# Optimization experiments

Hardware: AMD Instinct MI355X
Metric: run time of the kernel (lower is better)

The kernel has to match this reference:

```python
import jax, jax.numpy as jnp
import numpy as np

B, H, N, D, M = 1, 4, 2048, 64, 256  # batch, heads, seq, dim_heads, nb_features
EPS = 1e-4


def _gaussian_orthogonal_random_matrix(nb_rows, nb_cols, seed=0):
    # scaling=1 path of the torch code: stacked transposed-Q orthogonal blocks,
    # scaled by sqrt(nb_cols).
    rng = np.random.default_rng(seed)
    blocks = []
    for _ in range(nb_rows // nb_cols):
        q, _ = np.linalg.qr(rng.standard_normal((nb_cols, nb_cols)))
        blocks.append(q.T)
    final = np.concatenate(blocks, axis=0)  # [nb_rows, nb_cols]
    return jnp.asarray(np.sqrt(float(nb_cols)) * final, dtype=jnp.float32)


def setup_inputs() -> dict:
    key = jax.random.key(0)
    kq, kk, kv = jax.random.split(key, 3)
    return {
        "q": jax.random.normal(kq, (B, H, N, D), dtype=jnp.float32),
        "k": jax.random.normal(kk, (B, H, N, D), dtype=jnp.float32),
        "v": jax.random.normal(kv, (B, H, N, D), dtype=jnp.float32),
        "projection_matrix": _gaussian_orthogonal_random_matrix(M, D),
    }


def _softmax_kernel(data, projection_matrix, is_query):
    # data: [B,H,N,D], projection_matrix: [M,D] -> features [B,H,N,M]
    data_normalizer = 1.0 / data.shape[-1] ** 0.25
    ratio = 1.0 / projection_matrix.shape[0] ** 0.5
    data_dash = jnp.einsum("bhnd,md->bhnm", data_normalizer * data, projection_matrix)
    diag_data = jnp.sum(data * data, axis=-1) * 0.5 * data_normalizer ** 2  # [B,H,N]
    diag_data = diag_data[..., None]  # [B,H,N,1]
    if is_query:
        stab = jnp.max(data_dash, axis=-1, keepdims=True)
    else:
        stab = jnp.max(data_dash)
    return ratio * (jnp.exp(data_dash - diag_data - stab) + EPS)


def _causal_linear_attention(q, k, v):
    # q,k: [B,H,N,M] features; v: [B,H,N,E]
    k_cumsum = jnp.cumsum(k, axis=-2)                       # [B,H,N,M]
    context = jnp.einsum("bhnm,bhne->bhnme", k, v)          # outer products
    context = jnp.cumsum(context, axis=-3)                  # cumulative over n
    context = context / k_cumsum[..., None]                 # [B,H,N,M,E]
    return jnp.einsum("bhnme,bhnm->bhne", context, q)


def reference(q, k, v, projection_matrix):
    q_feat = _softmax_kernel(q, projection_matrix, is_query=True)
    k_feat = _softmax_kernel(k, projection_matrix, is_query=False)
    return _causal_linear_attention(q_feat, k_feat, v)
```

## Files before the change

kernel.cpp:

```cpp
#include <hip/hip_runtime.h>
#include <math.h>

#define NH   4
#define SEQ  2048
#define DH   64
#define NF   256
#define ROWS (NH*SEQ)
#define DN    0.35355339059327373f
#define DIAGC 0.0625f
#define RATIO 0.0625f
#define EPSF  1e-4f

typedef __attribute__((ext_vector_type(8))) short bf8;
typedef __attribute__((ext_vector_type(4))) short bf4;
typedef __attribute__((ext_vector_type(4))) float f4;

static __device__ __forceinline__ unsigned short f2bf(float x) {
  union { float f; unsigned u; } v; v.f = x;
  unsigned r = v.u + 0x7FFF + ((v.u >> 16) & 1);
  return (unsigned short)(r >> 16);
}
static __device__ __forceinline__ float bf2f(unsigned short b) {
  union { unsigned u; float f; } v; v.u = ((unsigned)b) << 16;
  return v.f;
}

__global__ __launch_bounds__(256) void k_proj(const float* __restrict__ q,
    const float* __restrict__ k, const float* __restrict__ v,
    const float* __restrict__ P,
    unsigned short* __restrict__ qfb, float* __restrict__ dshd,
    float* __restrict__ bmax, unsigned short* __restrict__ vtb) {
  __shared__ float lds[64*65];
  const int b = blockIdx.x;
  if (b >= 1024) {
    const int cb = b - 1024;
    const int h = cb >> 5, n0 = (cb & 31) * 64;
    const int tid = threadIdx.x;
    for (int i = tid; i < 4096; i += 256) {
      int n = i >> 6, e = i & 63;
      lds[n*65 + e] = v[((size_t)h*SEQ + n0 + n)*DH + e];
    }
    __syncthreads();
    for (int i = tid; i < 4096; i += 256) {
      int e = i >> 6, n = i & 63;
      vtb[((size_t)h*DH + e)*SEQ + n0 + n] = f2bf(lds[n*65 + e]);
    }
    return;
  }
  const bool isq = b < 512;
  const int tile = isq ? b : b - 512;
  const int w = threadIdx.x >> 6, lane = threadIdx.x & 63;
  const int lr = lane & 15, g = lane >> 4;
  const float* x = (isq ? q : k) + (size_t)tile*16*DH;

  f4 a  = *(const f4*)(x + lr*DH + g*8);
  f4 bb = *(const f4*)(x + lr*DH + g*8 + 4);
  f4 c  = *(const f4*)(x + lr*DH + 32 + g*8);
  f4 d  = *(const f4*)(x + lr*DH + 32 + g*8 + 4);
  float ss = 0.f;
#pragma unroll
  for (int i = 0; i < 4; ++i) ss += a[i]*a[i] + bb[i]*bb[i] + c[i]*c[i] + d[i]*d[i];
  ss += __shfl_xor(ss, 16);
  ss += __shfl_xor(ss, 32);

  bf8 xh0, xh1, xl0, xl1;
#pragma unroll
  for (int i = 0; i < 4; ++i) {
    float v0 = DN*a[i], v1 = DN*bb[i], v2 = DN*c[i], v3 = DN*d[i];
    unsigned short h0 = f2bf(v0), h1 = f2bf(v1), h2 = f2bf(v2), h3 = f2bf(v3);
    xh0[i] = (short)h0; xh0[i+4] = (short)h1;
    xh1[i] = (short)h2; xh1[i+4] = (short)h3;
    xl0[i]   = (short)f2bf(v0 - bf2f(h0)); xl0[i+4] = (short)f2bf(v1 - bf2f(h1));
    xl1[i]   = (short)f2bf(v2 - bf2f(h2)); xl1[i+4] = (short)f2bf(v3 - bf2f(h3));
  }

  const int ct0 = w*4;
  f4 dsh[4];
#pragma unroll
  for (int cc = 0; cc < 4; ++cc) {
    const int ct = ct0 + cc;
    const float* prow = P + (ct*16 + lr)*DH + g*8;
    f4 p0 = *(const f4*)(prow);
    f4 p1 = *(const f4*)(prow + 4);
    f4 p2 = *(const f4*)(prow + 32);
    f4 p3 = *(const f4*)(prow + 36);
    bf8 bh0, bl0, bh1, bl1;
#pragma unroll
    for (int i = 0; i < 4; ++i) {
      unsigned short h0 = f2bf(p0[i]), h1 = f2bf(p1[i]);
      unsigned short h2 = f2bf(p2[i]), h3 = f2bf(p3[i]);
      bh0[i] = (short)h0; bh0[i+4] = (short)h1;
      bh1[i] = (short)h2; bh1[i+4] = (short)h3;
      bl0[i]   = (short)f2bf(p0[i] - bf2f(h0)); bl0[i+4] = (short)f2bf(p1[i] - bf2f(h1));
      bl1[i]   = (short)f2bf(p2[i] - bf2f(h2)); bl1[i+4] = (short)f2bf(p3[i] - bf2f(h3));
    }
    f4 acc = {0.f, 0.f, 0.f, 0.f};
    acc = __builtin_amdgcn_mfma_f32_16x16x32_bf16(xh0, bh0, acc, 0, 0, 0);
    acc = __builtin_amdgcn_mfma_f32_16x16x32_bf16(xh1, bh1, acc, 0, 0, 0);
    acc = __builtin_amdgcn_mfma_f32_16x16x32_bf16(xh0, bl0, acc, 0, 0, 0);
    acc = __builtin_amdgcn_mfma_f32_16x16x32_bf16(xh1, bl1, acc, 0, 0, 0);
    acc = __builtin_amdgcn_mfma_f32_16x16x32_bf16(xl0, bh0, acc, 0, 0, 0);
    acc = __builtin_amdgcn_mfma_f32_16x16x32_bf16(xl1, bh1, acc, 0, 0, 0);
    dsh[cc] = acc;
  }

  f4 mr;
#pragma unroll
  for (int r = 0; r < 4; ++r)
    mr[r] = fmaxf(fmaxf(dsh[0][r], dsh[1][r]), fmaxf(dsh[2][r], dsh[3][r]));
#pragma unroll
  for (int mk = 1; mk <= 8; mk <<= 1) {
#pragma unroll
    for (int r = 0; r < 4; ++r) mr[r] = fmaxf(mr[r], __shfl_xor(mr[r], mk));
  }
  if (lr == 0) {
#pragma unroll
    for (int r = 0; r < 4; ++r) lds[w*16 + 4*g + r] = mr[r];
  }
  __syncthreads();
  float rm[4], sr[4];
#pragma unroll
  for (int r = 0; r < 4; ++r) {
    rm[r] = fmaxf(fmaxf(lds[0*16 + 4*g + r], lds[1*16 + 4*g + r]),
                  fmaxf(lds[2*16 + 4*g + r], lds[3*16 + 4*g + r]));
    sr[r] = __shfl(ss, 4*g + r);
  }

  if (isq) {
    unsigned short* ob = qfb + (size_t)tile*16*NF;
#pragma unroll
    for (int cc = 0; cc < 4; ++cc) {
#pragma unroll
      for (int r = 0; r < 4; ++r)
        ob[(4*g + r)*NF + (ct0 + cc)*16 + lr] =
            f2bf(RATIO*(expf(dsh[cc][r] - (sr[r]*DIAGC + rm[r])) + EPSF));
    }
  } else {
    float* db = dshd + (size_t)tile*16*NF;
#pragma unroll
    for (int cc = 0; cc < 4; ++cc) {
#pragma unroll
      for (int r = 0; r < 4; ++r)
        db[(4*g + r)*NF + (ct0 + cc)*16 + lr] = dsh[cc][r] - sr[r]*DIAGC;
    }
    if (w == 0 && lr == 0) {
#pragma unroll
      for (int r = 0; r < 4; ++r) bmax[tile*16 + 4*g + r] = mr[r];
    }
  }
}

__global__ __launch_bounds__(256) void k_feat2(const float* __restrict__ dshd,
    const float* __restrict__ bmax, unsigned short* __restrict__ kfb,
    unsigned short* __restrict__ kft, float* __restrict__ csum) {
  const int u = blockIdx.x, m = threadIdx.x;
  const int h = u >> 7, t = u & 127;
  __shared__ float red[256];
  float mx = -3.4e38f;
  for (int i = m; i < ROWS; i += 256) mx = fmaxf(mx, bmax[i]);
  red[m] = mx;
  __syncthreads();
  for (int s = 128; s > 0; s >>= 1) {
    if (m < s) red[m] = fmaxf(red[m], red[m+s]);
    __syncthreads();
  }
  const float gg = red[0];
  const float* db = dshd + (size_t)u*16*NF + m;
  unsigned short* ob = kfb + (size_t)u*16*NF + m;
  float run = 0.f;
  bf8 k0, k1;
#pragma unroll
  for (int r = 0; r < 16; ++r) {
    unsigned short bv = f2bf(RATIO*(expf(db[r*NF] - gg) + EPSF));
    ob[r*NF] = bv;
    if (r < 8) k0[r] = (short)bv; else k1[r-8] = (short)bv;
    run += bf2f(bv);
  }
  csum[(size_t)u*NF + m] = run;
  unsigned short* kt = kft + ((size_t)(h*NF + m))*SEQ + t*16;
  *(bf8*)kt = k0;
  *(bf8*)(kt + 8) = k1;
}

__global__ __launch_bounds__(64) void k_state_build(
    const unsigned short* __restrict__ vtb, const unsigned short* __restrict__ kft,
    float* __restrict__ stateP) {
  const int lane = threadIdx.x;
  const int lr = lane & 15, g = lane >> 4;
  const int c = blockIdx.x >> 2, mtg = blockIdx.x & 3;
  const int h = blockIdx.y;
  f4 acc[4][4];
#pragma unroll
  for (int et = 0; et < 4; ++et)
#pragma unroll
    for (int mt = 0; mt < 4; ++mt) acc[et][mt] = (f4){0.f,0.f,0.f,0.f};

#pragma unroll
  for (int ks = 0; ks < 4; ++ks) {
    const int j0 = c*128 + ks*32 + g*8;
    bf8 xv[4], ym[4];
#pragma unroll
    for (int et = 0; et < 4; ++et)
      xv[et] = *(const bf8*)(vtb + ((size_t)(h*DH + et*16 + lr))*SEQ + j0);
#pragma unroll
    for (int mt = 0; mt < 4; ++mt)
      ym[mt] = *(const bf8*)(kft + ((size_t)(h*NF + (4*mtg + mt)*16 + lr))*SEQ + j0);
#pragma unroll
    for (int et = 0; et < 4; ++et)
#pragma unroll
      for (int mt = 0; mt < 4; ++mt)
        acc[et][mt] = __builtin_amdgcn_mfma_f32_16x16x32_bf16(xv[et], ym[mt], acc[et][mt], 0, 0, 0);
  }
  float* sp = stateP + (size_t)(h*16 + c)*64*NF;
#pragma unroll
  for (int et = 0; et < 4; ++et)
#pragma unroll
    for (int mt = 0; mt < 4; ++mt)
#pragma unroll
      for (int r = 0; r < 4; ++r)
        sp[(size_t)(et*16 + 4*g + r)*NF + (4*mtg + mt)*16 + lr] = acc[et][mt][r];
}

__global__ __launch_bounds__(64) void k_state_scan(const float* __restrict__ stateP,
    unsigned short* __restrict__ sthi, unsigned short* __restrict__ stlo,
    float* __restrict__ csum) {
  const int h = blockIdx.y;
  if (blockIdx.x == 64) {
    const int m0 = threadIdx.x * 4;
    f4 run = {0.f, 0.f, 0.f, 0.f};
#pragma unroll 4
    for (int c = 0; c < 128; ++c) {
      float* p = csum + ((size_t)(h*128 + c))*NF + m0;
      f4 x = *(const f4*)p;
      *(f4*)p = run;
      run += x;
    }
    return;
  }
  const int e = blockIdx.x;
  const int m0 = threadIdx.x * 4;
  f4 run = {0.f, 0.f, 0.f, 0.f};
  for (int c = 0; c < 16; ++c) {
    const size_t idx = (size_t)((h*16 + c)*64 + e)*NF + m0;
    unsigned short hi[4], lo[4];
#pragma unroll
    for (int i = 0; i < 4; ++i) {
      hi[i] = f2bf(run[i]);
      lo[i] = f2bf(run[i] - bf2f(hi[i]));
    }
    *(bf4*)(sthi + idx) = *(bf4*)hi;
    *(bf4*)(stlo + idx) = *(bf4*)lo;
    run += *(const f4*)(stateP + idx);
  }
}

__global__ __launch_bounds__(128) void k_attn3(const unsigned short* __restrict__ qpb,
                                               const unsigned short* __restrict__ kfb,
                                               const unsigned short* __restrict__ vtb,
                                               const unsigned short* __restrict__ sthi,
                                               const unsigned short* __restrict__ stlo,
                                               const float* __restrict__ csum,
                                               float* __restrict__ out) {
  const int h = blockIdx.y;
  const int b = blockIdx.x;
  const int c = b >> 2, qt = b & 3;
  const int tid = threadIdx.x;
  const int wid = tid >> 6, lane = tid & 63;
  const int t = c*8 + qt*2 + wid;
  const int lr = lane & 15, g = lane >> 4;
  const int jc0 = c*8;
  const int nstage = qt*2 + 2;

  __shared__ __align__(16) char smem[26624];
  char* Ks = smem + 16384;
  char* Vs = smem + 24576;

  {
    const int u = h*128 + t;
    f4 run = *(const f4*)(csum + (size_t)u*NF + lane*4);
    const unsigned short* kfp = kfb + ((size_t)(h*SEQ + t*16))*NF + lane*4;
    const unsigned short* qfp = qpb + ((size_t)(h*SEQ + t*16))*NF + lane*4;
#pragma unroll
    for (int r = 0; r < 16; ++r) {
      bf4 kv = *(const bf4*)(kfp + (size_t)r*NF);
      bf4 qv = *(const bf4*)(qfp + (size_t)r*NF);
      unsigned short qp[4];
#pragma unroll
      for (int i = 0; i < 4; ++i) {
        run[i] += bf2f((unsigned short)kv[i]);
        qp[i] = f2bf(bf2f((unsigned short)qv[i]) / run[i]);
      }
      const int rloc = wid*16 + r;
      const int byte = (rloc*512 + lane*8) ^ ((rloc & 7) << 4);
      *(bf4*)(smem + byte) = *(bf4*)qp;
    }
  }
  __syncthreads();

  bf8 qf[8];
  {
    const int rloc = wid*16 + lr;
#pragma unroll
    for (int kb = 0; kb < 8; ++kb) {
      const int byte = (rloc*512 + g*16 + kb*64) ^ ((rloc & 7) << 4);
      qf[kb] = *(const bf8*)(smem + byte);
    }
  }

  const char* kTile = (const char*)(kfb + (size_t)h*SEQ*NF);
  const char* vTile = (const char*)(vtb + (size_t)h*DH*SEQ);

  const int ko0 = wid*4096 +    0 + lane*16;
  const int ko1 = wid*4096 + 1024 + lane*16;
  const int ko2 = wid*4096 + 2048 + lane*16;
  const int ko3 = wid*4096 + 3072 + lane*16;
  const int kw0 = ko0 ^ (((ko0 >> 9) & 7) << 4);
  const int kw1 = ko1 ^ (((ko1 >> 9) & 7) << 4);
  const int kw2 = ko2 ^ (((ko2 >> 9) & 7) << 4);
  const int kw3 = ko3 ^ (((ko3 >> 9) & 7) << 4);
  const int vo = tid*16;
  const int ve = vo >> 5;
  const int vn = vo & 31;

  f4 sk0, sk1, sk2, sk3, sv;
  {
    const char* kt = kTile + (size_t)jc0*8192;
    sk0 = *(const f4*)(kt + ko0);
    sk1 = *(const f4*)(kt + ko1);
    sk2 = *(const f4*)(kt + ko2);
    sk3 = *(const f4*)(kt + ko3);
    sv  = *(const f4*)(vTile + (size_t)ve*4096 + (size_t)jc0*32 + vn);
  }

  f4 o0 = {0,0,0,0}, o1 = {0,0,0,0}, o2 = {0,0,0,0}, o3 = {0,0,0,0};
  {
    const unsigned short* SH = sthi + ((size_t)((h*16 + c)*64 + lr))*NF + g*8;
    const unsigned short* SL = stlo + ((size_t)((h*16 + c)*64 + lr))*NF + g*8;
#pragma unroll
    for (int ks = 0; ks < 8; ++ks) {
#pragma unroll
      for (int et = 0; et < 4; ++et) {
        bf8 bh = *(const bf8*)(SH + et*16*NF + ks*32);
        bf8 bl = *(const bf8*)(SL + et*16*NF + ks*32);
        f4 acc = (et == 0) ? o0 : (et == 1) ? o1 : (et == 2) ? o2 : o3;
        acc = __builtin_amdgcn_mfma_f32_16x16x32_bf16(qf[ks], bh, acc, 0, 0, 0);
        acc = __builtin_amdgcn_mfma_f32_16x16x32_bf16(qf[ks], bl, acc, 0, 0, 0);
        if (et == 0) o0 = acc; else if (et == 1) o1 = acc; else if (et == 2) o2 = acc; else o3 = acc;
      }
    }
  }

  for (int jj = 0; jj < nstage; ++jj) {
    const int j = jc0 + jj;
    *(f4*)(Ks + kw0) = sk0;
    *(f4*)(Ks + kw1) = sk1;
    *(f4*)(Ks + kw2) = sk2;
    *(f4*)(Ks + kw3) = sk3;
    *(f4*)(Vs + vo) = sv;
    __syncthreads();
    if (jj + 1 < nstage) {
      const char* kt = kTile + (size_t)(j+1)*8192;
      sk0 = *(const f4*)(kt + ko0);
      sk1 = *(const f4*)(kt + ko1);
      sk2 = *(const f4*)(kt + ko2);
      sk3 = *(const f4*)(kt + ko3);
      sv  = *(const f4*)(vTile + (size_t)ve*4096 + (size_t)(j+1)*32 + vn);
    }
    if (j <= t) {
      bf8 kcs[8];
#pragma unroll
      for (int kb = 0; kb < 8; ++kb) {
        int off = (lr*512 + kb*64 + g*16) ^ ((lr & 7) << 4);
        kcs[kb] = *(const bf8*)(Ks + off);
      }
      f4 st = {0,0,0,0};
#pragma unroll
      for (int kb = 0; kb < 8; ++kb)
        st = __builtin_amdgcn_mfma_f32_16x16x32_bf16(kcs[kb], qf[kb], st, 0, 0, 0);
      if (j == t) {
#pragma unroll
        for (int rr = 0; rr < 4; ++rr) if (g*4 + rr > lr) st[rr] = 0.f;
      }
      bf8 sb = { (short)f2bf(st[0]), (short)f2bf(st[1]), (short)f2bf(st[2]), (short)f2bf(st[3]),
                 (short)0, (short)0, (short)0, (short)0 };
#pragma unroll
      for (int eb = 0; eb < 4; ++eb) {
        bf4 v4 = *(const bf4*)(Vs + (eb*16 + lr)*32 + g*8);
        bf8 vf = { v4[0], v4[1], v4[2], v4[3], (short)0, (short)0, (short)0, (short)0 };
        f4 acc = (eb == 0) ? o0 : (eb == 1) ? o1 : (eb == 2) ? o2 : o3;
        acc = __builtin_amdgcn_mfma_f32_16x16x32_bf16(sb, vf, acc, 0, 0, 0);
        if (eb == 0) o0 = acc; else if (eb == 1) o1 = acc; else if (eb == 2) o2 = acc; else o3 = acc;
      }
    }
    __syncthreads();
  }

  float* ob = out + ((size_t)(h*SEQ + t*16))*DH;
#pragma unroll
  for (int rr = 0; rr < 4; ++rr) {
    ob[(size_t)(4*g + rr)*DH +  0 + lr] = o0[rr];
    ob[(size_t)(4*g + rr)*DH + 16 + lr] = o1[rr];
    ob[(size_t)(4*g + rr)*DH + 32 + lr] = o2[rr];
    ob[(size_t)(4*g + rr)*DH + 48 + lr] = o3[rr];
  }
}

extern "C" void kernel_launch(void* const* d_in, const int* in_sizes, int n_in,
                              void* d_out, int out_size, void* d_ws, size_t ws_size,
                              hipStream_t stream) {
  const float* q = (const float*)d_in[0];
  const float* k = (const float*)d_in[1];
  const float* v = (const float*)d_in[2];
  const float* P = (const float*)d_in[3];
  float* out = (float*)d_out;

  char* ws = (char*)d_ws;
  unsigned short* qfb  = (unsigned short*)(ws);
  unsigned short* kfb  = (unsigned short*)(ws + (4u<<20));
  unsigned short* vtb  = (unsigned short*)(ws + (8u<<20));
  unsigned short* kft  = (unsigned short*)(ws + (12u<<20));
  float* dshd   = (float*)(ws + (16u<<20));
  float* bmax   = (float*)(ws + (24u<<20));
  float* csum   = (float*)(ws + (25u<<20));
  float* stateP = (float*)(ws + (28u<<20));
  unsigned short* sthi = (unsigned short*)(ws + (33u<<20));
  unsigned short* stlo = (unsigned short*)(ws + (36u<<20));

  k_proj       <<<1152, 256, 0, stream>>>(q, k, v, P, qfb, dshd, bmax, vtb);
  k_feat2      <<<512, 256, 0, stream>>>(dshd, bmax, kfb, kft, csum);
  k_state_build<<<dim3(64, NH), 64, 0, stream>>>(vtb, kft, stateP);
  k_state_scan <<<dim3(65, NH), 64, 0, stream>>>(stateP, sthi, stlo, csum);
  k_attn3      <<<dim3(64, NH), 128, 0, stream>>>(qfb, kfb, vtb, sthi, stlo, csum, out);
}
```

Before: 58.50 us.

## Fuse chunk state build and prefix scan into one MFMA accumulation kernel

Replaces the separate per-chunk state-build kernel and the scan kernel with a single kernel. Each block owns one 16x16 (e,m) tile and accumulates MFMA products across all chunks sequentially, writing the exclusive prefix as hi/lo bf16 before each chunk. This removes one launch and the fp32 stateP round trip through memory. The cost is a longer serial dependency chain per block: 64 MFMAs and 16 chunk-sized loads each. The csum scan is folded into the same launch as extra blocks.

```diff
diff --git a/kernel.cpp b/kernel.cpp
--- a/kernel.cpp
+++ b/kernel.cpp
@@ -182,50 +182,13 @@
   *(bf8*)(kt + 8) = k1;
 }
 
-__global__ __launch_bounds__(64) void k_state_build(
+__global__ __launch_bounds__(64) void k_state(
     const unsigned short* __restrict__ vtb, const unsigned short* __restrict__ kft,
-    float* __restrict__ stateP) {
-  const int lane = threadIdx.x;
-  const int lr = lane & 15, g = lane >> 4;
-  const int c = blockIdx.x >> 2, mtg = blockIdx.x & 3;
-  const int h = blockIdx.y;
-  f4 acc[4][4];
-#pragma unroll
-  for (int et = 0; et < 4; ++et)
-#pragma unroll
-    for (int mt = 0; mt < 4; ++mt) acc[et][mt] = (f4){0.f,0.f,0.f,0.f};
-
-#pragma unroll
-  for (int ks = 0; ks < 4; ++ks) {
-    const int j0 = c*128 + ks*32 + g*8;
-    bf8 xv[4], ym[4];
-#pragma unroll
-    for (int et = 0; et < 4; ++et)
-      xv[et] = *(const bf8*)(vtb + ((size_t)(h*DH + et*16 + lr))*SEQ + j0);
-#pragma unroll
-    for (int mt = 0; mt < 4; ++mt)
-      ym[mt] = *(const bf8*)(kft + ((size_t)(h*NF + (4*mtg + mt)*16 + lr))*SEQ + j0);
-#pragma unroll
-    for (int et = 0; et < 4; ++et)
-#pragma unroll
-      for (int mt = 0; mt < 4; ++mt)
-        acc[et][mt] = __builtin_amdgcn_mfma_f32_16x16x32_bf16(xv[et], ym[mt], acc[et][mt], 0, 0, 0);
-  }
-  float* sp = stateP + (size_t)(h*16 + c)*64*NF;
-#pragma unroll
-  for (int et = 0; et < 4; ++et)
-#pragma unroll
-    for (int mt = 0; mt < 4; ++mt)
-#pragma unroll
-      for (int r = 0; r < 4; ++r)
-        sp[(size_t)(et*16 + 4*g + r)*NF + (4*mtg + mt)*16 + lr] = acc[et][mt][r];
-}
-
-__global__ __launch_bounds__(64) void k_state_scan(const float* __restrict__ stateP,
     unsigned short* __restrict__ sthi, unsigned short* __restrict__ stlo,
     float* __restrict__ csum) {
-  const int h = blockIdx.y;
-  if (blockIdx.x == 64) {
+  const int bx = blockIdx.x;
+  if (bx >= 256) {
+    const int h = bx - 256;
     const int m0 = threadIdx.x * 4;
     f4 run = {0.f, 0.f, 0.f, 0.f};
 #pragma unroll 4
@@ -237,20 +200,29 @@
     }
     return;
   }
-  const int e = blockIdx.x;
-  const int m0 = threadIdx.x * 4;
-  f4 run = {0.f, 0.f, 0.f, 0.f};
+  const int lane = threadIdx.x;
+  const int lr = lane & 15, g = lane >> 4;
+  const int h = bx >> 6, et = (bx >> 4) & 3, mt = bx & 15;
+
+  const unsigned short* vb = vtb + ((size_t)(h*DH + et*16 + lr))*SEQ;
+  const unsigned short* kb = kft + ((size_t)(h*NF + mt*16 + lr))*SEQ;
+
+  f4 cum = {0.f, 0.f, 0.f, 0.f};
   for (int c = 0; c < 16; ++c) {
-    const size_t idx = (size_t)((h*16 + c)*64 + e)*NF + m0;
-    unsigned short hi[4], lo[4];
-#pragma unroll
-    for (int i = 0; i < 4; ++i) {
-      hi[i] = f2bf(run[i]);
-      lo[i] = f2bf(run[i] - bf2f(hi[i]));
-    }
-    *(bf4*)(sthi + idx) = *(bf4*)hi;
-    *(bf4*)(stlo + idx) = *(bf4*)lo;
-    run += *(const f4*)(stateP + idx);
+    const size_t base = ((size_t)((h*16 + c)*64 + et*16 + 4*g))*NF + mt*16 + lr;
+#pragma unroll
+    for (int r = 0; r < 4; ++r) {
+      unsigned short hi = f2bf(cum[r]);
+      sthi[base + (size_t)r*NF] = hi;
+      stlo[base + (size_t)r*NF] = f2bf(cum[r] - bf2f(hi));
+    }
+#pragma unroll
+    for (int ks = 0; ks < 4; ++ks) {
+      const int j0 = c*128 + ks*32 + g*8;
+      bf8 xv = *(const bf8*)(vb + j0);
+      bf8 ym = *(const bf8*)(kb + j0);
+      cum = __builtin_amdgcn_mfma_f32_16x16x32_bf16(xv, ym, cum, 0, 0, 0);
+    }
   }
 }
 
@@ -422,13 +394,11 @@
   float* dshd   = (float*)(ws + (16u<<20));
   float* bmax   = (float*)(ws + (24u<<20));
   float* csum   = (float*)(ws + (25u<<20));
-  float* stateP = (float*)(ws + (28u<<20));
   unsigned short* sthi = (unsigned short*)(ws + (33u<<20));
   unsigned short* stlo = (unsigned short*)(ws + (36u<<20));
 
-  k_proj       <<<1152, 256, 0, stream>>>(q, k, v, P, qfb, dshd, bmax, vtb);
-  k_feat2      <<<512, 256, 0, stream>>>(dshd, bmax, kfb, kft, csum);
-  k_state_build<<<dim3(64, NH), 64, 0, stream>>>(vtb, kft, stateP);
-  k_state_scan <<<dim3(65, NH), 64, 0, stream>>>(stateP, sthi, stlo, csum);
-  k_attn3      <<<dim3(64, NH), 128, 0, stream>>>(qfb, kfb, vtb, sthi, stlo, csum, out);
-}
+  k_proj  <<<1152, 256, 0, stream>>>(q, k, v, P, qfb, dshd, bmax, vtb);
+  k_feat2 <<<512, 256, 0, stream>>>(dshd, bmax, kfb, kft, csum);
+  k_state <<<260, 64, 0, stream>>>(vtb, kft, sthi, stlo, csum);
+  k_attn3 <<<dim3(64, NH), 128, 0, stream>>>(qfb, kfb, vtb, sthi, stlo, csum, out);
+}
```

After: 57.88 us. Within noise of the previous version (-1.1%).
